# Kernel tuning notes

Hardware: AMD Instinct MI355X
Metric: run time of the kernel (lower is better)

Reference implementation:

```python
import jax, jax.numpy as jnp
import numpy as np

TRIM = 0.2
BIG = jnp.float32(1e30)  # sentinel pushing invalid pixels to the sorted tail


def setup_inputs() -> dict:
    key = jax.random.key(0)
    k1, k2, k3 = jax.random.split(key, 3)
    B, H, W = 32, 480, 640
    prediction = jax.random.normal(k1, (B, H, W), dtype=jnp.float32)
    target = jax.random.normal(k2, (B, H, W), dtype=jnp.float32)
    mask = jax.random.randint(k3, (B, H, W), 0, 2).astype(jnp.int32)
    return {"prediction": prediction, "target": target, "mask": mask}


def reference(prediction, target, mask):
    maskb = mask.astype(bool)
    M_total = jnp.sum(maskb)  # total number of valid pixels (== M.sum() in torch)
    abs_res = jnp.abs(prediction - target)
    # invalid pixels -> BIG so they sort to the end and are trimmed away
    flat = jnp.where(maskb, abs_res, BIG).reshape(-1)
    sorted_res = jnp.sort(flat)
    # keep the smallest int(num_valid * (1 - trim)) residuals
    k = jnp.floor(M_total.astype(jnp.float32) * (1.0 - TRIM)).astype(jnp.int32)
    keep = jnp.arange(flat.shape[0]) < k
    batch_loss = jnp.sum(jnp.where(keep, sorted_res, jnp.float32(0.0)))
    denom = 2.0 * M_total.astype(jnp.float32)
    # guard against fully-invalid mask (torch returns 0.0 in that case)
    return jnp.where(M_total > 0, batch_loss / jnp.maximum(denom, 1.0), jnp.float32(0.0))
```

## Files before the change

kernel.cpp:

```cpp
#include <hip/hip_runtime.h>

#define THREADS 256
#define NSUB 8
#define NBLK 960
#define NBINS 256
#define RPER 16
#define RBLK (NBLK / RPER)
#define QSCALE 32768.0f
#define MASK40 ((1ull << 40) - 1ull)


__global__ __launch_bounds__(THREADS) void k_hist(
    const float* __restrict__ pred, const float* __restrict__ targ,
    const int* __restrict__ mask, unsigned long long* __restrict__ hist_part,
    unsigned long long* __restrict__ fcnt, unsigned long long* __restrict__ fq,
    int N)
{
  __shared__ unsigned long long lh[NSUB][NBINS];
  for (int i = threadIdx.x; i < NSUB * NBINS; i += THREADS)
    ((unsigned long long*)lh)[i] = 0ull;
  if (blockIdx.x == 0) {
    for (int i = threadIdx.x; i < NBINS; i += THREADS) { fcnt[i] = 0ull; fq[i] = 0ull; }
  }
  __syncthreads();

  const int sub  = threadIdx.x >> 5;
  const int gtid = blockIdx.x * THREADS + threadIdx.x;
  const int gsz  = gridDim.x * THREADS;
  const int n4   = N >> 2;

  auto acc = [&](float pv, float tv, int valid) {
    if (valid) {
      const float r = fabsf(pv - tv);
      const unsigned int b = (unsigned int)fminf(r * 32.0f, 255.0f);
      const unsigned long long q =
          (unsigned long long)(unsigned int)(fminf(r, 8.0f) * QSCALE + 0.5f);
      atomicAdd(&lh[sub][b], (1ull << 40) | q);
    }
  };

  const float4* p4 = (const float4*)pred;
  const float4* t4 = (const float4*)targ;
  const int4*   m4 = (const int4*)mask;

#define CONSUME(P, T, M)                                        \
  do {                                                          \
    acc((P).x, (T).x, (M).x); acc((P).y, (T).y, (M).y);         \
    acc((P).z, (T).z, (M).z); acc((P).w, (T).w, (M).w);         \
  } while (0)

  const int steps = n4 / gsz;
  if (steps * gsz == n4 && steps >= 2) {
    float4 pA = p4[gtid],       tA = t4[gtid];       int4 mA = m4[gtid];
    float4 pB = p4[gtid + gsz], tB = t4[gtid + gsz]; int4 mB = m4[gtid + gsz];
    int s = 0;
    for (; s + 3 < steps; s += 2) {
      CONSUME(pA, tA, mA);
      { const int i = gtid + (s + 2) * gsz; pA = p4[i]; tA = t4[i]; mA = m4[i]; }
      CONSUME(pB, tB, mB);
      { const int i = gtid + (s + 3) * gsz; pB = p4[i]; tB = t4[i]; mB = m4[i]; }
    }
    CONSUME(pA, tA, mA);
    CONSUME(pB, tB, mB);
    for (int r = s + 2; r < steps; ++r) {
      const int i = gtid + r * gsz;
      const float4 p = p4[i]; const float4 t = t4[i]; const int4 m = m4[i];
      CONSUME(p, t, m);
    }
  } else {
    for (int i = gtid; i < n4; i += gsz) {
      const float4 p = p4[i]; const float4 t = t4[i]; const int4 m = m4[i];
      CONSUME(p, t, m);
    }
  }
  for (int i = (n4 << 2) + gtid; i < N; i += gsz)
    acc(pred[i], targ[i], mask[i]);
#undef CONSUME

  __syncthreads();
  const int t = threadIdx.x;
  unsigned long long v = 0ull;
#pragma unroll
  for (int c = 0; c < NSUB; ++c) v += lh[c][t];
  hist_part[(size_t)blockIdx.x * NBINS + t] = v;
}

__global__ __launch_bounds__(THREADS) void k_reduce(
    const unsigned long long* __restrict__ hist_part,
    unsigned long long* __restrict__ fcnt, unsigned long long* __restrict__ fq)
{
  const int t = threadIdx.x;
  unsigned long long c = 0ull, q = 0ull;
  const int base = blockIdx.x * RPER;
  for (int p = base; p < base + RPER; ++p) {
    const unsigned long long v = hist_part[(size_t)p * NBINS + t];
    c += v >> 40;
    q += v & MASK40;
  }
  if (c) atomicAdd(&fcnt[t], c);
  if (q) atomicAdd(&fq[t], q);
}

__global__ __launch_bounds__(THREADS) void k_final(
    const unsigned long long* __restrict__ fcnt,
    const unsigned long long* __restrict__ fq, float* __restrict__ out)
{
  __shared__ unsigned long long sc[NBINS];
  __shared__ unsigned long long sq[NBINS];
  const int t = threadIdx.x;
  sc[t] = fcnt[t];
  sq[t] = fq[t];
  __syncthreads();
  if (t == 0) {
    unsigned long long M64 = 0ull;
    for (int b = 0; b < NBINS; ++b) M64 += sc[b];
    float res = 0.f;
    if (M64 > 0ull) {
      const unsigned int M = (unsigned int)M64;
      const unsigned int k = (unsigned int)floorf((float)M * 0.8f);
      if (k > 0u) {
        unsigned long long cum = 0ull, qbelow = 0ull;
        int tb = NBINS - 1;
        for (int b = 0; b < NBINS; ++b) {
          const unsigned long long c = sc[b];
          if (cum + c >= (unsigned long long)k) { tb = b; break; }
          cum += c;
          qbelow += sq[b];
        }
        double sum_below = (double)qbelow / (double)QSCALE;
        const unsigned long long cnt_tb = sc[tb];
        if ((unsigned long long)k > cum && cnt_tb > 0ull) {
          const double mean_tb = ((double)sq[tb] / (double)QSCALE) / (double)cnt_tb;
          sum_below += (double)(k - (unsigned int)cum) * mean_tb;
        }
        double denom = 2.0 * (double)M;
        if (denom < 1.0) denom = 1.0;
        res = (float)(sum_below / denom);
      }
    }
    out[0] = res;
  }
}

extern "C" void kernel_launch(void* const* d_in, const int* in_sizes, int n_in,
                              void* d_out, int out_size, void* d_ws, size_t ws_size,
                              hipStream_t stream)
{
  const float* pred = (const float*)d_in[0];
  const float* targ = (const float*)d_in[1];
  const int*   mask = (const int*)d_in[2];
  float* out = (float*)d_out;
  const int N = in_sizes[0];

  char* ws = (char*)d_ws;
  unsigned long long* fcnt      = (unsigned long long*)ws;
  unsigned long long* fq        = (unsigned long long*)(ws + 2048);
  unsigned long long* hist_part = (unsigned long long*)(ws + 8192);

  k_hist  <<<NBLK, THREADS, 0, stream>>>(pred, targ, mask, hist_part, fcnt, fq, N);
  k_reduce<<<RBLK, THREADS, 0, stream>>>(hist_part, fcnt, fq);
  k_final <<<1,    THREADS, 0, stream>>>(fcnt, fq, out);
}
```

Baseline: 34.75 us.

## Fuse reduce and final kernels via ticket, deepen nontemporal load pipeline

The separate reduce and final kernels become one: the last block to take an atomic ticket computes the trimmed-sum result, which removes one kernel launch. The main histogram loop is fully unrolled for a fixed step count with a three-deep register prefetch ring and nontemporal loads, aiming to keep more memory requests in flight and avoid polluting the cache. This adds register pressure and a specialized path that only applies when the input size matches the step count exactly.

```diff
diff --git a/kernel.cpp b/kernel.cpp
--- a/kernel.cpp
+++ b/kernel.cpp
@@ -1,8 +1,12 @@
 #include <hip/hip_runtime.h>
+
+typedef float nfloat4 __attribute__((ext_vector_type(4)));
+typedef int   nint4   __attribute__((ext_vector_type(4)));
 
 #define THREADS 256
 #define NSUB 8
 #define NBLK 960
+#define STEPS 10
 #define NBINS 256
 #define RPER 16
 #define RBLK (NBLK / RPER)
@@ -10,17 +14,25 @@
 #define MASK40 ((1ull << 40) - 1ull)
 
 
+__device__ __forceinline__ nfloat4 ntl_f4(const float* p) {
+  return __builtin_nontemporal_load((const nfloat4*)p);
+}
+__device__ __forceinline__ nint4 ntl_i4(const int* p) {
+  return __builtin_nontemporal_load((const nint4*)p);
+}
+
 __global__ __launch_bounds__(THREADS) void k_hist(
     const float* __restrict__ pred, const float* __restrict__ targ,
     const int* __restrict__ mask, unsigned long long* __restrict__ hist_part,
     unsigned long long* __restrict__ fcnt, unsigned long long* __restrict__ fq,
-    int N)
+    unsigned int* __restrict__ ticket, int N)
 {
   __shared__ unsigned long long lh[NSUB][NBINS];
   for (int i = threadIdx.x; i < NSUB * NBINS; i += THREADS)
     ((unsigned long long*)lh)[i] = 0ull;
   if (blockIdx.x == 0) {
     for (int i = threadIdx.x; i < NBINS; i += THREADS) { fcnt[i] = 0ull; fq[i] = 0ull; }
+    if (threadIdx.x == 0) *ticket = 0u;
   }
   __syncthreads();
 
@@ -39,35 +51,37 @@
     }
   };
 
-  const float4* p4 = (const float4*)pred;
-  const float4* t4 = (const float4*)targ;
-  const int4*   m4 = (const int4*)mask;
-
 #define CONSUME(P, T, M)                                        \
   do {                                                          \
     acc((P).x, (T).x, (M).x); acc((P).y, (T).y, (M).y);         \
     acc((P).z, (T).z, (M).z); acc((P).w, (T).w, (M).w);         \
   } while (0)
 
-  const int steps = n4 / gsz;
-  if (steps * gsz == n4 && steps >= 2) {
-    float4 pA = p4[gtid],       tA = t4[gtid];       int4 mA = m4[gtid];
-    float4 pB = p4[gtid + gsz], tB = t4[gtid + gsz]; int4 mB = m4[gtid + gsz];
-    int s = 0;
-    for (; s + 3 < steps; s += 2) {
-      CONSUME(pA, tA, mA);
-      { const int i = gtid + (s + 2) * gsz; pA = p4[i]; tA = t4[i]; mA = m4[i]; }
-      CONSUME(pB, tB, mB);
-      { const int i = gtid + (s + 3) * gsz; pB = p4[i]; tB = t4[i]; mB = m4[i]; }
+  if (n4 == gsz * STEPS) {
+    nfloat4 P[3], T[3];
+    nint4   Mv[3];
+#pragma unroll
+    for (int u = 0; u < 3; ++u) {
+      const int i = gtid + u * gsz;
+      P[u] = ntl_f4(pred + 4 * (size_t)i);
+      T[u] = ntl_f4(targ + 4 * (size_t)i);
+      Mv[u] = ntl_i4(mask + 4 * (size_t)i);
     }
-    CONSUME(pA, tA, mA);
-    CONSUME(pB, tB, mB);
-    for (int r = s + 2; r < steps; ++r) {
-      const int i = gtid + r * gsz;
-      const float4 p = p4[i]; const float4 t = t4[i]; const int4 m = m4[i];
-      CONSUME(p, t, m);
+#pragma unroll
+    for (int s = 0; s < STEPS; ++s) {
+      const int slot = s % 3;
+      CONSUME(P[slot], T[slot], Mv[slot]);
+      if (s + 3 < STEPS) {
+        const int i = gtid + (s + 3) * gsz;
+        P[slot] = ntl_f4(pred + 4 * (size_t)i);
+        T[slot] = ntl_f4(targ + 4 * (size_t)i);
+        Mv[slot] = ntl_i4(mask + 4 * (size_t)i);
+      }
     }
   } else {
+    const float4* p4 = (const float4*)pred;
+    const float4* t4 = (const float4*)targ;
+    const int4*   m4 = (const int4*)mask;
     for (int i = gtid; i < n4; i += gsz) {
       const float4 p = p4[i]; const float4 t = t4[i]; const int4 m = m4[i];
       CONSUME(p, t, m);
@@ -85,29 +99,34 @@
   hist_part[(size_t)blockIdx.x * NBINS + t] = v;
 }
 
-__global__ __launch_bounds__(THREADS) void k_reduce(
+__global__ __launch_bounds__(THREADS) void k_reduce_final(
     const unsigned long long* __restrict__ hist_part,
-    unsigned long long* __restrict__ fcnt, unsigned long long* __restrict__ fq)
+    unsigned long long* __restrict__ fcnt, unsigned long long* __restrict__ fq,
+    unsigned int* __restrict__ ticket, float* __restrict__ out)
 {
   const int t = threadIdx.x;
-  unsigned long long c = 0ull, q = 0ull;
-  const int base = blockIdx.x * RPER;
-  for (int p = base; p < base + RPER; ++p) {
-    const unsigned long long v = hist_part[(size_t)p * NBINS + t];
-    c += v >> 40;
-    q += v & MASK40;
+  {
+    unsigned long long c = 0ull, q = 0ull;
+    const int base = blockIdx.x * RPER;
+    for (int p = base; p < base + RPER; ++p) {
+      const unsigned long long v = hist_part[(size_t)p * NBINS + t];
+      c += v >> 40;
+      q += v & MASK40;
+    }
+    if (c) atomicAdd(&fcnt[t], c);
+    if (q) atomicAdd(&fq[t], q);
   }
-  if (c) atomicAdd(&fcnt[t], c);
-  if (q) atomicAdd(&fq[t], q);
-}
 
-__global__ __launch_bounds__(THREADS) void k_final(
-    const unsigned long long* __restrict__ fcnt,
-    const unsigned long long* __restrict__ fq, float* __restrict__ out)
-{
+  __threadfence();
+  __syncthreads();
+  __shared__ unsigned int amLast;
+  if (t == 0) amLast = (atomicAdd(ticket, 1u) == (unsigned int)(RBLK - 1)) ? 1u : 0u;
+  __syncthreads();
+  if (!amLast) return;
+  __threadfence();
+
   __shared__ unsigned long long sc[NBINS];
   __shared__ unsigned long long sq[NBINS];
-  const int t = threadIdx.x;
   sc[t] = fcnt[t];
   sq[t] = fq[t];
   __syncthreads();
@@ -155,9 +174,9 @@
   char* ws = (char*)d_ws;
   unsigned long long* fcnt      = (unsigned long long*)ws;
   unsigned long long* fq        = (unsigned long long*)(ws + 2048);
+  unsigned int*       ticket    = (unsigned int*)(ws + 4096);
   unsigned long long* hist_part = (unsigned long long*)(ws + 8192);
 
-  k_hist  <<<NBLK, THREADS, 0, stream>>>(pred, targ, mask, hist_part, fcnt, fq, N);
-  k_reduce<<<RBLK, THREADS, 0, stream>>>(hist_part, fcnt, fq);
-  k_final <<<1,    THREADS, 0, stream>>>(fcnt, fq, out);
+  k_hist        <<<NBLK, THREADS, 0, stream>>>(pred, targ, mask, hist_part, fcnt, fq, ticket, N);
+  k_reduce_final<<<RBLK, THREADS, 0, stream>>>(hist_part, fcnt, fq, ticket, out);
 }
```

After: 37.69 us. 1.08x slower.

## Replace full-data histogram with sampled threshold estimate and atomic-free sum pass

Applied to the files above, without the earlier changes.

A small 16-block pre-pass builds a fine histogram from a strided sample of the data, and its last block picks an estimated 80th-percentile threshold. The main pass then streams all pixels with no shared-memory atomics. It accumulates in registers the quantized sum and count of valid residuals below the threshold, plus the valid count, and reduces them per block. The final kernel fills the gap between the kept count and k with the threshold value. This removes the per-element 64-bit LDS atomics of the old histogram. The price is an extra launch and memset, plus accuracy that now depends on how well the sample estimates the quantile.

```diff
diff --git a/kernel.cpp b/kernel.cpp
--- a/kernel.cpp
+++ b/kernel.cpp
@@ -1,53 +1,115 @@
 #include <hip/hip_runtime.h>
 
 #define THREADS 256
-#define NSUB 8
-#define NBLK 960
-#define NBINS 256
-#define RPER 16
-#define RBLK (NBLK / RPER)
-#define QSCALE 32768.0f
-#define MASK40 ((1ull << 40) - 1ull)
-
-
-__global__ __launch_bounds__(THREADS) void k_hist(
+#define SBLK 16
+#define SBINS 2048
+#define NBLK 1920
+#define QSCALE 8192.0f
+#define RCAP 64.0f
+
+
+struct Ctrl { float That; unsigned int msample; unsigned int pad[6]; };
+
+__global__ __launch_bounds__(THREADS) void k_sample(
     const float* __restrict__ pred, const float* __restrict__ targ,
-    const int* __restrict__ mask, unsigned long long* __restrict__ hist_part,
-    unsigned long long* __restrict__ fcnt, unsigned long long* __restrict__ fq,
-    int N)
-{
-  __shared__ unsigned long long lh[NSUB][NBINS];
-  for (int i = threadIdx.x; i < NSUB * NBINS; i += THREADS)
-    ((unsigned long long*)lh)[i] = 0ull;
-  if (blockIdx.x == 0) {
-    for (int i = threadIdx.x; i < NBINS; i += THREADS) { fcnt[i] = 0ull; fq[i] = 0ull; }
-  }
-  __syncthreads();
-
-  const int sub  = threadIdx.x >> 5;
-  const int gtid = blockIdx.x * THREADS + threadIdx.x;
-  const int gsz  = gridDim.x * THREADS;
-  const int n4   = N >> 2;
+    const int* __restrict__ mask, unsigned int* __restrict__ shist,
+    unsigned int* __restrict__ ticket, Ctrl* __restrict__ ctrl, int N)
+{
+  __shared__ unsigned int lh[SBINS];
+  __shared__ unsigned int s1[THREADS];
+  __shared__ unsigned int lval;
+  for (int i = threadIdx.x; i < SBINS; i += THREADS) lh[i] = 0u;
+  if (threadIdx.x == 0) lval = 0u;
+  __syncthreads();
+
+  const int n4 = N >> 2;
+  const int nchunk = n4 >> 6;
+  const int lane = threadIdx.x & 63;
+  const int wid  = (blockIdx.x * THREADS + threadIdx.x) >> 6;
+  const int nw   = (SBLK * THREADS) >> 6;
+  unsigned int myval = 0;
 
   auto acc = [&](float pv, float tv, int valid) {
     if (valid) {
       const float r = fabsf(pv - tv);
-      const unsigned int b = (unsigned int)fminf(r * 32.0f, 255.0f);
-      const unsigned long long q =
-          (unsigned long long)(unsigned int)(fminf(r, 8.0f) * QSCALE + 0.5f);
-      atomicAdd(&lh[sub][b], (1ull << 40) | q);
+      const unsigned int b = (unsigned int)fminf(r * 256.0f, 2047.0f);
+      atomicAdd(&lh[b], 1u);
+      ++myval;
     }
   };
-
-  const float4* p4 = (const float4*)pred;
-  const float4* t4 = (const float4*)targ;
-  const int4*   m4 = (const int4*)mask;
-
+  for (int c = wid; c * 256 < nchunk; c += nw) {
+    const int g = c * 256 * 64 + lane;
+    const float4 p = ((const float4*)pred)[g];
+    const float4 t = ((const float4*)targ)[g];
+    const int4   m = ((const int4*)mask)[g];
+    acc(p.x, t.x, m.x); acc(p.y, t.y, m.y); acc(p.z, t.z, m.z); acc(p.w, t.w, m.w);
+  }
+  atomicAdd(&lval, myval);
+  __syncthreads();
+  for (int i = threadIdx.x; i < SBINS; i += THREADS)
+    if (lh[i]) atomicAdd(&shist[i], lh[i]);
+  if (threadIdx.x == 0 && lval) atomicAdd(&ctrl->msample, lval);
+
+  __threadfence();
+  __syncthreads();
+  __shared__ unsigned int amLast;
+  if (threadIdx.x == 0) amLast = (atomicAdd(ticket, 1u) == SBLK - 1) ? 1u : 0u;
+  __syncthreads();
+  if (!amLast) return;
+  __threadfence();
+
+  for (int i = threadIdx.x; i < SBINS; i += THREADS) lh[i] = shist[i];
+  __syncthreads();
+  unsigned int cs = 0;
+#pragma unroll
+  for (int j = 0; j < SBINS / THREADS; ++j) cs += lh[threadIdx.x * (SBINS / THREADS) + j];
+  s1[threadIdx.x] = cs;
+  __syncthreads();
+  if (threadIdx.x == 0) {
+    const unsigned int ms = ctrl->msample;
+    float That = RCAP;
+    if (ms > 0u) {
+      const float goal = 0.8f * (float)ms;
+      unsigned int cum = 0; int c = 0;
+      for (; c < THREADS; ++c) { if ((float)(cum + s1[c]) >= goal) break; cum += s1[c]; }
+      if (c >= THREADS) c = THREADS - 1;
+      const int per = SBINS / THREADS;
+      int b = c * per;
+      for (; b < c * per + per; ++b) { if ((float)(cum + lh[b]) >= goal) break; cum += lh[b]; }
+      if (b >= c * per + per) b = c * per + per - 1;
+      That = (b >= SBINS - 1) ? RCAP : (float)(b + 1) * (1.0f / 256.0f);
+    }
+    ctrl->That = That;
+  }
+}
+
+__global__ __launch_bounds__(THREADS) void k_main(
+    const float* __restrict__ pred, const float* __restrict__ targ,
+    const int* __restrict__ mask, const Ctrl* __restrict__ ctrl,
+    uint4* __restrict__ part, int N)
+{
+  const float That = ctrl->That;
+  unsigned int q = 0u, cl = 0u, mv = 0u;
+
+  auto acc = [&](float pv, float tv, int valid) {
+    if (valid) {
+      ++mv;
+      const float r = fabsf(pv - tv);
+      if (r < That) { ++cl; q += (unsigned int)(fminf(r, RCAP) * QSCALE + 0.5f); }
+    }
+  };
 #define CONSUME(P, T, M)                                        \
   do {                                                          \
     acc((P).x, (T).x, (M).x); acc((P).y, (T).y, (M).y);         \
     acc((P).z, (T).z, (M).z); acc((P).w, (T).w, (M).w);         \
   } while (0)
+
+  const int gtid = blockIdx.x * THREADS + threadIdx.x;
+  const int gsz  = gridDim.x * THREADS;
+  const int n4   = N >> 2;
+  const float4* p4 = (const float4*)pred;
+  const float4* t4 = (const float4*)targ;
+  const int4*   m4 = (const int4*)mask;
 
   const int steps = n4 / gsz;
   if (steps * gsz == n4 && steps >= 2) {
@@ -77,65 +139,51 @@
     acc(pred[i], targ[i], mask[i]);
 #undef CONSUME
 
-  __syncthreads();
+  __shared__ unsigned int rq[THREADS], rc[THREADS], rm[THREADS];
+  rq[threadIdx.x] = q; rc[threadIdx.x] = cl; rm[threadIdx.x] = mv;
+  __syncthreads();
+  for (int s = THREADS >> 1; s > 0; s >>= 1) {
+    if (threadIdx.x < s) {
+      rq[threadIdx.x] += rq[threadIdx.x + s];
+      rc[threadIdx.x] += rc[threadIdx.x + s];
+      rm[threadIdx.x] += rm[threadIdx.x + s];
+    }
+    __syncthreads();
+  }
+  if (threadIdx.x == 0)
+    part[blockIdx.x] = make_uint4(rq[0], rc[0], rm[0], 0u);
+}
+
+__global__ __launch_bounds__(THREADS) void k_final(
+    const uint4* __restrict__ part, const Ctrl* __restrict__ ctrl,
+    float* __restrict__ out)
+{
+  __shared__ unsigned long long sQ[THREADS], sC[THREADS], sM[THREADS];
   const int t = threadIdx.x;
-  unsigned long long v = 0ull;
-#pragma unroll
-  for (int c = 0; c < NSUB; ++c) v += lh[c][t];
-  hist_part[(size_t)blockIdx.x * NBINS + t] = v;
-}
-
-__global__ __launch_bounds__(THREADS) void k_reduce(
-    const unsigned long long* __restrict__ hist_part,
-    unsigned long long* __restrict__ fcnt, unsigned long long* __restrict__ fq)
-{
-  const int t = threadIdx.x;
-  unsigned long long c = 0ull, q = 0ull;
-  const int base = blockIdx.x * RPER;
-  for (int p = base; p < base + RPER; ++p) {
-    const unsigned long long v = hist_part[(size_t)p * NBINS + t];
-    c += v >> 40;
-    q += v & MASK40;
-  }
-  if (c) atomicAdd(&fcnt[t], c);
-  if (q) atomicAdd(&fq[t], q);
-}
-
-__global__ __launch_bounds__(THREADS) void k_final(
-    const unsigned long long* __restrict__ fcnt,
-    const unsigned long long* __restrict__ fq, float* __restrict__ out)
-{
-  __shared__ unsigned long long sc[NBINS];
-  __shared__ unsigned long long sq[NBINS];
-  const int t = threadIdx.x;
-  sc[t] = fcnt[t];
-  sq[t] = fq[t];
-  __syncthreads();
+  unsigned long long Q = 0ull, C = 0ull, M = 0ull;
+  for (int i = t; i < NBLK; i += THREADS) {
+    const uint4 v = part[i];
+    Q += v.x; C += v.y; M += v.z;
+  }
+  sQ[t] = Q; sC[t] = C; sM[t] = M;
+  __syncthreads();
+  for (int s = THREADS >> 1; s > 0; s >>= 1) {
+    if (t < s) { sQ[t] += sQ[t + s]; sC[t] += sC[t + s]; sM[t] += sM[t + s]; }
+    __syncthreads();
+  }
   if (t == 0) {
-    unsigned long long M64 = 0ull;
-    for (int b = 0; b < NBINS; ++b) M64 += sc[b];
+    const unsigned long long Mtot = sM[0];
     float res = 0.f;
-    if (M64 > 0ull) {
-      const unsigned int M = (unsigned int)M64;
-      const unsigned int k = (unsigned int)floorf((float)M * 0.8f);
+    if (Mtot > 0ull) {
+      const unsigned int Mu = (unsigned int)Mtot;
+      const unsigned int k = (unsigned int)floorf((float)Mu * 0.8f);
       if (k > 0u) {
-        unsigned long long cum = 0ull, qbelow = 0ull;
-        int tb = NBINS - 1;
-        for (int b = 0; b < NBINS; ++b) {
-          const unsigned long long c = sc[b];
-          if (cum + c >= (unsigned long long)k) { tb = b; break; }
-          cum += c;
-          qbelow += sq[b];
-        }
-        double sum_below = (double)qbelow / (double)QSCALE;
-        const unsigned long long cnt_tb = sc[tb];
-        if ((unsigned long long)k > cum && cnt_tb > 0ull) {
-          const double mean_tb = ((double)sq[tb] / (double)QSCALE) / (double)cnt_tb;
-          sum_below += (double)(k - (unsigned int)cum) * mean_tb;
-        }
-        double denom = 2.0 * (double)M;
+        const double That = (double)ctrl->That;
+        const double sum = (double)sQ[0] / (double)QSCALE
+                         + ((double)k - (double)sC[0]) * That;
+        double denom = 2.0 * (double)Mu;
         if (denom < 1.0) denom = 1.0;
-        res = (float)(sum_below / denom);
+        res = (float)(sum / denom);
       }
     }
     out[0] = res;
@@ -153,11 +201,14 @@
   const int N = in_sizes[0];
 
   char* ws = (char*)d_ws;
-  unsigned long long* fcnt      = (unsigned long long*)ws;
-  unsigned long long* fq        = (unsigned long long*)(ws + 2048);
-  unsigned long long* hist_part = (unsigned long long*)(ws + 8192);
-
-  k_hist  <<<NBLK, THREADS, 0, stream>>>(pred, targ, mask, hist_part, fcnt, fq, N);
-  k_reduce<<<RBLK, THREADS, 0, stream>>>(hist_part, fcnt, fq);
-  k_final <<<1,    THREADS, 0, stream>>>(fcnt, fq, out);
-}
+  Ctrl*         ctrl   = (Ctrl*)ws;
+  unsigned int* shist  = (unsigned int*)(ws + 256);
+  unsigned int* ticket = (unsigned int*)(ws + 8448);
+  uint4*        part   = (uint4*)(ws + 16384);
+
+  hipMemsetAsync(d_ws, 0, 12288, stream);
+
+  k_sample<<<SBLK, THREADS, 0, stream>>>(pred, targ, mask, shist, ticket, ctrl, N);
+  k_main  <<<NBLK, THREADS, 0, stream>>>(pred, targ, mask, ctrl, part, N);
+  k_final <<<1,    THREADS, 0, stream>>>(part, ctrl, out);
+}
```

Result: slower. 44.92 us (+29.3%).
